# Kernel tuning notes

Measured on AMD Instinct MI355X. Metric: run time of the kernel, lower is better.

The kernel has to match this reference:

```python
import jax, jax.numpy as jnp
import numpy as np

HID = 2048
HEADS = 16
HD = HID // HEADS  # 128


def setup_inputs() -> dict:
    key = jax.random.key(0)
    ks = jax.random.split(key, 9)
    s = 0.02
    return {
        "hidden_state": jax.random.normal(ks[0], (2, 2048, HID), dtype=jnp.float32),
        "Wq": jax.random.normal(ks[1], (HID, HID), dtype=jnp.float32) * s,
        "bq": jnp.zeros((HID,), dtype=jnp.float32),
        "Wk": jax.random.normal(ks[2], (HID, HD), dtype=jnp.float32) * s,
        "bk": jnp.zeros((HD,), dtype=jnp.float32),
        "Wv": jax.random.normal(ks[3], (HID, HD), dtype=jnp.float32) * s,
        "bv": jnp.zeros((HD,), dtype=jnp.float32),
        "Wo": jax.random.normal(ks[4], (HID, HID), dtype=jnp.float32) * s,
        "bo": jnp.zeros((HID,), dtype=jnp.float32),
    }


def reference(hidden_state, Wq, bq, Wk, bk, Wv, bv, Wo, bo):
    bs, seq, _ = hidden_state.shape
    # Q: [b, s, H, hd] -> per-head; K,V: single shared head [b, s, hd]
    q = (hidden_state @ Wq + bq).reshape(bs, seq, HEADS, HD)
    k = hidden_state @ Wk + bk  # [b, s, hd]
    v = hidden_state @ Wv + bv  # [b, s, hd]
    scale = 1.0 / jnp.sqrt(jnp.float32(HD))
    # scores: [b, h, s_q, s_k] against shared K head
    scores = jnp.einsum("bqhd,bkd->bhqk", q, k) * scale
    attn = jax.nn.softmax(scores, axis=-1)
    out = jnp.einsum("bhqk,bkd->bqhd", attn, v)  # [b, s, h, hd]
    out = out.reshape(bs, seq, HID)
    return out @ Wo + bo
```

## Files before the change

### kernel.cpp

```cpp
#include <hip/hip_runtime.h>
#include <math.h>

#define HIDN 2048
#define NHEADS 16
#define HDIM 128
#define SEQ 2048
#define NB 2

#define C2 0.12751744154f

typedef __bf16 bf16x8 __attribute__((ext_vector_type(8)));
typedef float f32x4 __attribute__((ext_vector_type(4)));

__device__ __forceinline__ unsigned short f32_to_bf16(float f) {
  unsigned int u = __float_as_uint(f);
  u += 0x7FFFu + ((u >> 16) & 1u);
  return (unsigned short)(u >> 16);
}

__device__ __forceinline__ unsigned pack_bf16x2(float a, float b) {
  return (unsigned)f32_to_bf16(a) | ((unsigned)f32_to_bf16(b) << 16);
}

__device__ __forceinline__ unsigned pack_bf16x2_trunc(float a, float b) {
  return __builtin_amdgcn_perm(__float_as_uint(b), __float_as_uint(a), 0x07060302u);
}

__device__ __forceinline__ void gload_lds16(const void* g, void* l) {
  __builtin_amdgcn_global_load_lds(
      (__attribute__((address_space(1))) void*)(g),
      (__attribute__((address_space(3))) void*)(l), 16, 0, 0);
}

__global__ __launch_bounds__(256) void cast_f32_bf16(
    const float* __restrict__ in, unsigned short* __restrict__ out, int n4) {
  int i = blockIdx.x * blockDim.x + threadIdx.x;
  if (i >= n4) return;
  float4 v = ((const float4*)in)[i];
  ushort4 o;
  o.x = f32_to_bf16(v.x); o.y = f32_to_bf16(v.y);
  o.z = f32_to_bf16(v.z); o.w = f32_to_bf16(v.w);
  ((ushort4*)out)[i] = o;
}

__global__ __launch_bounds__(256) void wtrans_big(
    const float* __restrict__ wq, unsigned short* __restrict__ dq,
    const float* __restrict__ wo, unsigned short* __restrict__ do_) {
  __shared__ float tile[32][33];
  const float* src = blockIdx.z ? wo : wq;
  unsigned short* dst = blockIdx.z ? do_ : dq;
  const float m = blockIdx.z ? 1.0f : C2;
  int c0 = blockIdx.x * 32, r0 = blockIdx.y * 32;
  int tx = threadIdx.x & 31, ty = threadIdx.x >> 5;
#pragma unroll
  for (int i = 0; i < 32; i += 8)
    tile[ty + i][tx] = src[(size_t)(r0 + ty + i) * 2048 + c0 + tx];
  __syncthreads();
#pragma unroll
  for (int i = 0; i < 32; i += 8)
    dst[(size_t)(c0 + ty + i) * 2048 + r0 + tx] = f32_to_bf16(tile[tx][ty + i] * m);
}

__global__ __launch_bounds__(256) void wtrans_small(
    const float* __restrict__ wk, const float* __restrict__ wv,
    unsigned short* __restrict__ dk, unsigned short* __restrict__ dv,
    const float* __restrict__ bq, const float* __restrict__ bk,
    const float* __restrict__ bv, float* __restrict__ biasout) {
  __shared__ float tile[32][33];
  const float* src = blockIdx.z ? wv : wk;
  unsigned short* dst = blockIdx.z ? dv : dk;
  int c0 = blockIdx.x * 32, r0 = blockIdx.y * 32;
  int tx = threadIdx.x & 31, ty = threadIdx.x >> 5;
#pragma unroll
  for (int i = 0; i < 32; i += 8)
    tile[ty + i][tx] = src[(size_t)(r0 + ty + i) * 128 + c0 + tx];
  __syncthreads();
#pragma unroll
  for (int i = 0; i < 32; i += 8)
    dst[(size_t)(c0 + ty + i) * 2048 + r0 + tx] = f32_to_bf16(tile[tx][ty + i]);
  if (blockIdx.z == 0) {
    int lb = blockIdx.y * 4 + blockIdx.x;
    if (lb < 9) {
      int i = lb * 256 + threadIdx.x;
      if (i < 2304)
        biasout[i] = (i < 2048) ? bq[i] * C2
                                : ((i < 2176) ? bk[i - 2048] : bv[i - 2176]);
    }
  }
}

__global__ __launch_bounds__(256) void vtrans(
    const unsigned short* __restrict__ qkv, unsigned short* __restrict__ vt) {
  __shared__ unsigned short tile[32][33];
  const unsigned short* src = qkv + (size_t)blockIdx.z * SEQ * 2304 + 2176;
  unsigned short* dst = vt + (size_t)blockIdx.z * 128 * SEQ;
  int c0 = blockIdx.x * 32, r0 = blockIdx.y * 32;
  int tx = threadIdx.x & 31, ty = threadIdx.x >> 5;
#pragma unroll
  for (int i = 0; i < 32; i += 8)
    tile[ty + i][tx] = src[(size_t)(r0 + ty + i) * 2304 + c0 + tx];
  __syncthreads();
  const int s = r0 + tx;
  const int col = (s & ~63) | (((s >> 5) & 1) * 32 + ((s >> 2) & 3) * 8 +
                               ((s >> 4) & 1) * 4 + (s & 3));
#pragma unroll
  for (int i = 0; i < 32; i += 8)
    dst[(size_t)(c0 + ty + i) * SEQ + col] = tile[tx][ty + i];
}

template <int BN>
__global__ __launch_bounds__(256) void gemm_bt(
    const unsigned short* __restrict__ A,
    const unsigned short* __restrict__ BT,
    const float* __restrict__ bias,
    void* __restrict__ C, int K, int ldc, int outBf16) {
  constexpr int NT = BN / 32;
  __shared__ unsigned short As[128 * 64];
  __shared__ unsigned short Bs[BN * 64];
  const int tid = threadIdx.x;
  const int lane = tid & 63;
  const int wave = tid >> 6;
  const int wr = wave >> 1, wc = wave & 1;
  const int ml = lane & 15, quad = lane >> 4;
  const long bm = (long)blockIdx.x * 128;
  const long bn = (long)blockIdx.y * BN;

  const f32x4 zero4 = {0.f, 0.f, 0.f, 0.f};
  f32x4 acc[4][NT];
#pragma unroll
  for (int mt = 0; mt < 4; ++mt)
#pragma unroll
    for (int nt = 0; nt < NT; ++nt) acc[mt][nt] = zero4;

  const int srow = lane >> 3;
  const int scol = ((lane & 7) ^ srow) * 8;

  for (int k0 = 0; k0 < K; k0 += 64) {
    __syncthreads();
#pragma unroll
    for (int r = 0; r < 4; ++r) {
      const int rowb = r * 32 + wave * 8;
      gload_lds16(A + (bm + rowb + srow) * (long)K + k0 + scol, &As[rowb * 64]);
    }
#pragma unroll
    for (int r = 0; r < NT; ++r) {
      const int rowb = r * 32 + wave * 8;
      gload_lds16(BT + (bn + rowb + srow) * (long)K + k0 + scol, &Bs[rowb * 64]);
    }
    __syncthreads();
#pragma unroll
    for (int kk = 0; kk < 64; kk += 32) {
      const int g0 = (kk >> 3) + quad;
      bf16x8 af[4], bf[NT];
#pragma unroll
      for (int mt = 0; mt < 4; ++mt)
        af[mt] = *(const bf16x8*)&As[(wr * 64 + mt * 16 + ml) * 64 +
                                     ((g0 ^ (ml & 7)) << 3)];
#pragma unroll
      for (int nt = 0; nt < NT; ++nt)
        bf[nt] = *(const bf16x8*)&Bs[(wc * (BN / 2) + nt * 16 + ml) * 64 +
                                     ((g0 ^ (ml & 7)) << 3)];
#pragma unroll
      for (int mt = 0; mt < 4; ++mt)
#pragma unroll
        for (int nt = 0; nt < NT; ++nt)
          acc[mt][nt] = __builtin_amdgcn_mfma_f32_16x16x32_bf16(
              af[mt], bf[nt], acc[mt][nt], 0, 0, 0);
    }
  }

#pragma unroll
  for (int mt = 0; mt < 4; ++mt) {
#pragma unroll
    for (int nt = 0; nt < NT; ++nt) {
      const long col = bn + wc * (BN / 2) + nt * 16 + ml;
      const float bval = bias ? bias[col] : 0.f;
#pragma unroll
      for (int r = 0; r < 4; ++r) {
        const long row = bm + wr * 64 + mt * 16 + quad * 4 + r;
        const float v = acc[mt][nt][r] + bval;
        if (outBf16)
          ((unsigned short*)C)[row * ldc + col] = f32_to_bf16(v);
        else
          ((float*)C)[row * ldc + col] = v;
      }
    }
  }
}

__global__ __launch_bounds__(256, 2) void mqa_attn(
    const unsigned short* __restrict__ qkv,
    const unsigned short* __restrict__ vt,
    unsigned short* __restrict__ outp) {
  __shared__ unsigned short Ks[2][64 * 128];
  __shared__ unsigned short VTs[2][128 * 64];

  const int lane = threadIdx.x & 63;
  const int wave = threadIdx.x >> 6;
  const int ml = lane & 15, quad = lane >> 4;
  const int h = blockIdx.y, b = blockIdx.z;
  const long q0 = (long)blockIdx.x * 128;
  const long base = (long)b * SEQ;

  bf16x8 aq[2][4];
#pragma unroll
  for (int n = 0; n < 2; ++n) {
    const unsigned short* qrow =
        qkv + (base + q0 + wave * 32 + n * 16 + ml) * 2304 + h * 128;
#pragma unroll
    for (int ks = 0; ks < 4; ++ks)
      aq[n][ks] = *(const bf16x8*)(qrow + ks * 32 + quad * 8);
  }

  const f32x4 zero4 = {0.f, 0.f, 0.f, 0.f};
  f32x4 o[8][2];
#pragma unroll
  for (int mt2 = 0; mt2 < 8; ++mt2)
#pragma unroll
    for (int n = 0; n < 2; ++n) o[mt2][n] = zero4;
  f32x4 o9[2] = {zero4, zero4};

  bf16x8 ones_af;
  {
    union { unsigned u[4]; bf16x8 v; } cv;
    const unsigned w = (ml == 0) ? 0x3F803F80u : 0u;
    cv.u[0] = w; cv.u[1] = w; cv.u[2] = w; cv.u[3] = w;
    ones_af = cv.v;
  }

  const int srowK = lane >> 4;
  const int scolK = ((lane & 15) ^ (wave * 4 + srowK)) * 8;
  const int srowV = lane >> 3;
  const int scolV = ((lane & 7) ^ srowV) * 8;
  const unsigned short* kp = qkv + (base + srowK) * 2304 + 2048 + scolK;
  const unsigned short* vp = vt + ((long)b * 128 + srowV) * SEQ + scolV;

  auto stage = [&](int buf, int ktn) {
    const unsigned short* kpp = kp + (long)ktn * (64 * 2304);
    const unsigned short* vpp = vp + ktn * 64;
#pragma unroll
    for (int r = 0; r < 4; ++r) {
      const int rowb = r * 16 + wave * 4;
      gload_lds16(kpp + (long)rowb * 2304, &Ks[buf][rowb * 128]);
    }
#pragma unroll
    for (int r = 0; r < 4; ++r) {
      const int rowb = r * 32 + wave * 8;
      gload_lds16(vpp + (long)rowb * SEQ, &VTs[buf][rowb * 64]);
    }
  };

  stage(0, 0);

  for (int kt = 0; kt < SEQ / 64; ++kt) {
    const int cur = kt & 1;
    __syncthreads();
    if (kt < SEQ / 64 - 1) stage(cur ^ 1, kt + 1);

    f32x4 s[4][2];
#pragma unroll
    for (int mt = 0; mt < 4; ++mt)
#pragma unroll
      for (int n = 0; n < 2; ++n) s[mt][n] = zero4;
#pragma unroll
    for (int ks = 0; ks < 4; ++ks) {
#pragma unroll
      for (int mt = 0; mt < 4; ++mt) {
        bf16x8 ak = *(const bf16x8*)&Ks[cur][(mt * 16 + ml) * 128 +
                                            (((ks * 4 + quad) ^ ml) << 3)];
#pragma unroll
        for (int n = 0; n < 2; ++n)
          s[mt][n] = __builtin_amdgcn_mfma_f32_16x16x32_bf16(
              ak, aq[n][ks], s[mt][n], 0, 0, 0);
      }
    }

    unsigned pk[2][4][2];
#pragma unroll
    for (int mt = 0; mt < 4; ++mt)
#pragma unroll
      for (int n = 0; n < 2; ++n) {
        const float p0 = __builtin_amdgcn_exp2f(s[mt][n][0]);
        const float p1 = __builtin_amdgcn_exp2f(s[mt][n][1]);
        const float p2 = __builtin_amdgcn_exp2f(s[mt][n][2]);
        const float p3 = __builtin_amdgcn_exp2f(s[mt][n][3]);
        pk[n][mt][0] = pack_bf16x2_trunc(p0, p1);
        pk[n][mt][1] = pack_bf16x2_trunc(p2, p3);
      }

#pragma unroll
    for (int ks2 = 0; ks2 < 2; ++ks2) {
      bf16x8 bp[2];
#pragma unroll
      for (int n = 0; n < 2; ++n) {
        union { unsigned u[4]; bf16x8 v; } cv;
        cv.u[0] = pk[n][2 * ks2][0];
        cv.u[1] = pk[n][2 * ks2][1];
        cv.u[2] = pk[n][2 * ks2 + 1][0];
        cv.u[3] = pk[n][2 * ks2 + 1][1];
        bp[n] = cv.v;
      }
#pragma unroll
      for (int n = 0; n < 2; ++n)
        o9[n] = __builtin_amdgcn_mfma_f32_16x16x32_bf16(
            ones_af, bp[n], o9[n], 0, 0, 0);
#pragma unroll
      for (int mt2 = 0; mt2 < 8; ++mt2) {
        bf16x8 av = *(const bf16x8*)&VTs[cur][(mt2 * 16 + ml) * 64 +
                                             (((ks2 * 4 + quad) ^ (ml & 7)) << 3)];
#pragma unroll
        for (int n = 0; n < 2; ++n)
          o[mt2][n] = __builtin_amdgcn_mfma_f32_16x16x32_bf16(
              av, bp[n], o[mt2][n], 0, 0, 0);
      }
    }
  }

  float inv[2];
#pragma unroll
  for (int n = 0; n < 2; ++n)
    inv[n] = 1.f / __shfl(o9[n][0], ml);

#pragma unroll
  for (int n = 0; n < 2; ++n) {
    const long row = base + q0 + wave * 32 + n * 16 + ml;
#pragma unroll
    for (int mt2 = 0; mt2 < 8; ++mt2) {
      uint2 w;
      w.x = pack_bf16x2(o[mt2][n][0] * inv[n], o[mt2][n][1] * inv[n]);
      w.y = pack_bf16x2(o[mt2][n][2] * inv[n], o[mt2][n][3] * inv[n]);
      *(uint2*)&outp[row * HIDN + h * HDIM + mt2 * 16 + quad * 4] = w;
    }
  }
}

extern "C" void kernel_launch(void* const* d_in, const int* in_sizes, int n_in,
                              void* d_out, int out_size, void* d_ws, size_t ws_size,
                              hipStream_t stream) {
  const float* hidden = (const float*)d_in[0];
  const float* Wq = (const float*)d_in[1];
  const float* bq = (const float*)d_in[2];
  const float* Wk = (const float*)d_in[3];
  const float* bk = (const float*)d_in[4];
  const float* Wv = (const float*)d_in[5];
  const float* bv = (const float*)d_in[6];
  const float* Wo = (const float*)d_in[7];
  const float* bo = (const float*)d_in[8];
  float* out = (float*)d_out;

  char* ws = (char*)d_ws;
  const size_t MB = 1u << 20;
  unsigned short* hb    = (unsigned short*)(ws);
  unsigned short* attn  = hb;
  unsigned short* wqkvT = (unsigned short*)(ws + 16 * MB);
  unsigned short* woT   = (unsigned short*)(ws + 25 * MB);
  unsigned short* qkv   = (unsigned short*)(ws + 33 * MB);
  unsigned short* vt    = (unsigned short*)(ws + 51 * MB);
  float* biasqkv        = (float*)(ws + 52 * MB);

  cast_f32_bf16<<<8192, 256, 0, stream>>>(hidden, hb, (NB * SEQ * HIDN) / 4);
  wtrans_big<<<dim3(64, 64, 2), 256, 0, stream>>>(Wq, wqkvT, Wo, woT);
  wtrans_small<<<dim3(4, 64, 2), 256, 0, stream>>>(
      Wk, Wv, wqkvT + (size_t)2048 * 2048, wqkvT + (size_t)2176 * 2048,
      bq, bk, bv, biasqkv);

  gemm_bt<96><<<dim3(32, 24), 256, 0, stream>>>(hb, wqkvT, biasqkv, qkv, 2048, 2304, 1);

  vtrans<<<dim3(4, 64, 2), 256, 0, stream>>>(qkv, vt);

  mqa_attn<<<dim3(SEQ / 128, NHEADS, NB), 256, 0, stream>>>(qkv, vt, attn);

  gemm_bt<128><<<dim3(32, 16), 256, 0, stream>>>(attn, woT, bo, out, 2048, 2048, 0);
}
```

Before: 280.4 us.

## Replace GEMM with 256x256 double-buffered pipelined MFMA kernel with grid swizzle

Swaps the single-buffered 128xBN GEMM for a 512-thread, 256x256-tile kernel. It double-buffers LDS and interleaves global-to-LDS loads for the next k-tile with MFMA work on the current one, using explicit waitcnt, barriers and setprio. It also remaps block IDs for XCD-aware locality. The larger tiles cut global traffic per FLOP, but the grid drops to 144/128 blocks on a 256-CU device, so many CUs sit idle and LDS use per block goes up.

```diff
diff --git a/kernel.cpp b/kernel.cpp
--- a/kernel.cpp
+++ b/kernel.cpp
@@ -108,81 +108,156 @@
     dst[(size_t)(c0 + ty + i) * SEQ + col] = tile[tx][ty + i];
 }
 
-template <int BN>
-__global__ __launch_bounds__(256) void gemm_bt(
+template <int NBY, int LDC, int OUTBF16>
+__global__ __launch_bounds__(512, 2) void gemm256(
     const unsigned short* __restrict__ A,
     const unsigned short* __restrict__ BT,
     const float* __restrict__ bias,
-    void* __restrict__ C, int K, int ldc, int outBf16) {
-  constexpr int NT = BN / 32;
-  __shared__ unsigned short As[128 * 64];
-  __shared__ unsigned short Bs[BN * 64];
+    void* __restrict__ C, int K) {
+  __shared__ unsigned short As[2][256 * 64];
+  __shared__ unsigned short Bs[2][256 * 64];
   const int tid = threadIdx.x;
   const int lane = tid & 63;
   const int wave = tid >> 6;
-  const int wr = wave >> 1, wc = wave & 1;
+  const int wr = wave >> 2;
+  const int wc = wave & 3;
   const int ml = lane & 15, quad = lane >> 4;
-  const long bm = (long)blockIdx.x * 128;
-  const long bn = (long)blockIdx.y * BN;
+
+  const int orig = blockIdx.x;
+  const int qx = gridDim.x >> 3;
+  const int lid = (orig & 7) * qx + (orig >> 3);
+  const long bm = (long)(lid / NBY) * 256;
+  const long bn = (long)(lid % NBY) * 256;
+
+  const int srow = tid >> 3;
+  const int scol = ((tid & 7) ^ (srow & 7)) * 8;
+  const unsigned short* Ag = A + (bm + srow) * (long)K + scol;
+  const unsigned short* Bg = BT + (bn + srow) * (long)K + scol;
 
   const f32x4 zero4 = {0.f, 0.f, 0.f, 0.f};
-  f32x4 acc[4][NT];
-#pragma unroll
-  for (int mt = 0; mt < 4; ++mt)
-#pragma unroll
-    for (int nt = 0; nt < NT; ++nt) acc[mt][nt] = zero4;
-
-  const int srow = lane >> 3;
-  const int scol = ((lane & 7) ^ srow) * 8;
-
-  for (int k0 = 0; k0 < K; k0 += 64) {
-    __syncthreads();
-#pragma unroll
-    for (int r = 0; r < 4; ++r) {
-      const int rowb = r * 32 + wave * 8;
-      gload_lds16(A + (bm + rowb + srow) * (long)K + k0 + scol, &As[rowb * 64]);
-    }
-#pragma unroll
-    for (int r = 0; r < NT; ++r) {
-      const int rowb = r * 32 + wave * 8;
-      gload_lds16(BT + (bn + rowb + srow) * (long)K + k0 + scol, &Bs[rowb * 64]);
-    }
-    __syncthreads();
-#pragma unroll
-    for (int kk = 0; kk < 64; kk += 32) {
-      const int g0 = (kk >> 3) + quad;
-      bf16x8 af[4], bf[NT];
-#pragma unroll
-      for (int mt = 0; mt < 4; ++mt)
-        af[mt] = *(const bf16x8*)&As[(wr * 64 + mt * 16 + ml) * 64 +
-                                     ((g0 ^ (ml & 7)) << 3)];
-#pragma unroll
-      for (int nt = 0; nt < NT; ++nt)
-        bf[nt] = *(const bf16x8*)&Bs[(wc * (BN / 2) + nt * 16 + ml) * 64 +
-                                     ((g0 ^ (ml & 7)) << 3)];
-#pragma unroll
-      for (int mt = 0; mt < 4; ++mt)
-#pragma unroll
-        for (int nt = 0; nt < NT; ++nt)
-          acc[mt][nt] = __builtin_amdgcn_mfma_f32_16x16x32_bf16(
-              af[mt], bf[nt], acc[mt][nt], 0, 0, 0);
-    }
-  }
-
-#pragma unroll
-  for (int mt = 0; mt < 4; ++mt) {
-#pragma unroll
-    for (int nt = 0; nt < NT; ++nt) {
-      const long col = bn + wc * (BN / 2) + nt * 16 + ml;
+  f32x4 acc[8][4];
+#pragma unroll
+  for (int mt = 0; mt < 8; ++mt)
+#pragma unroll
+    for (int nt = 0; nt < 4; ++nt) acc[mt][nt] = zero4;
+
+  bf16x8 bfr[4][2];
+
+#define STA(buf, koff, R0) \
+  gload_lds16(Ag + (long)(R0) * K + (koff), &As[buf][((R0) + 8 * wave) * 64])
+#define STB(buf, koff, R0) \
+  gload_lds16(Bg + (long)(R0) * K + (koff), &Bs[buf][((R0) + 8 * wave) * 64])
+#define RDA(buf, mt, kk) \
+  (*(const bf16x8*)&As[buf][(wr * 128 + (mt) * 16 + ml) * 64 + \
+                            ((((kk) * 4 + quad) ^ (ml & 7)) << 3)])
+#define RDB(buf, nt, kk) \
+  (*(const bf16x8*)&Bs[buf][(wc * 64 + (nt) * 16 + ml) * 64 + \
+                            ((((kk) * 4 + quad) ^ (ml & 7)) << 3)])
+
+  STB(0, 0, 0); STB(0, 0, 64); STB(0, 0, 128); STB(0, 0, 192);
+  STA(0, 0, 0); STA(0, 0, 128); STA(0, 0, 64); STA(0, 0, 192);
+  asm volatile("s_waitcnt vmcnt(2)" ::: "memory");
+  __builtin_amdgcn_s_barrier();
+
+  const int NT = K >> 6;
+  for (int t = 0; t < NT - 1; ++t) {
+    const int buf = t & 1, nbuf = buf ^ 1;
+    const long kn = (long)(t + 1) << 6;
+#pragma unroll
+    for (int q = 0; q < 4; ++q) {
+      __builtin_amdgcn_sched_barrier(0);
+      bf16x8 afr[2][2];
+      if (q == 0) {
+#pragma unroll
+        for (int nt = 0; nt < 4; ++nt)
+#pragma unroll
+          for (int kk = 0; kk < 2; ++kk) bfr[nt][kk] = RDB(buf, nt, kk);
+      }
+#pragma unroll
+      for (int j = 0; j < 2; ++j)
+#pragma unroll
+        for (int kk = 0; kk < 2; ++kk) afr[j][kk] = RDA(buf, 2 * q + j, kk);
+      if (q == 0) { STB(nbuf, kn, 0); STB(nbuf, kn, 64); }
+      if (q == 1) {
+        STB(nbuf, kn, 128); STB(nbuf, kn, 192);
+        asm volatile("s_waitcnt vmcnt(4)" ::: "memory");
+      }
+      if (q == 2) { STA(nbuf, kn, 0); STA(nbuf, kn, 128); }
+      if (q == 3) {
+        STA(nbuf, kn, 64); STA(nbuf, kn, 192);
+        asm volatile("s_waitcnt vmcnt(2)" ::: "memory");
+      }
+      __builtin_amdgcn_sched_barrier(0);
+      __builtin_amdgcn_s_barrier();
+      __builtin_amdgcn_sched_barrier(0);
+      __builtin_amdgcn_s_setprio(1);
+#pragma unroll
+      for (int j = 0; j < 2; ++j)
+#pragma unroll
+        for (int nt = 0; nt < 4; ++nt)
+#pragma unroll
+          for (int kk = 0; kk < 2; ++kk)
+            acc[2 * q + j][nt] = __builtin_amdgcn_mfma_f32_16x16x32_bf16(
+                afr[j][kk], bfr[nt][kk], acc[2 * q + j][nt], 0, 0, 0);
+      __builtin_amdgcn_s_setprio(0);
+      __builtin_amdgcn_sched_barrier(0);
+      __builtin_amdgcn_s_barrier();
+    }
+  }
+
+  {
+    const int buf = (NT - 1) & 1;
+#pragma unroll
+    for (int q = 0; q < 4; ++q) {
+      __builtin_amdgcn_sched_barrier(0);
+      bf16x8 afr[2][2];
+      if (q == 0) {
+#pragma unroll
+        for (int nt = 0; nt < 4; ++nt)
+#pragma unroll
+          for (int kk = 0; kk < 2; ++kk) bfr[nt][kk] = RDB(buf, nt, kk);
+      }
+#pragma unroll
+      for (int j = 0; j < 2; ++j)
+#pragma unroll
+        for (int kk = 0; kk < 2; ++kk) afr[j][kk] = RDA(buf, 2 * q + j, kk);
+      if (q == 1) asm volatile("s_waitcnt vmcnt(0)" ::: "memory");
+      __builtin_amdgcn_sched_barrier(0);
+      __builtin_amdgcn_s_barrier();
+      __builtin_amdgcn_sched_barrier(0);
+      __builtin_amdgcn_s_setprio(1);
+#pragma unroll
+      for (int j = 0; j < 2; ++j)
+#pragma unroll
+        for (int nt = 0; nt < 4; ++nt)
+#pragma unroll
+          for (int kk = 0; kk < 2; ++kk)
+            acc[2 * q + j][nt] = __builtin_amdgcn_mfma_f32_16x16x32_bf16(
+                afr[j][kk], bfr[nt][kk], acc[2 * q + j][nt], 0, 0, 0);
+      __builtin_amdgcn_s_setprio(0);
+      __builtin_amdgcn_sched_barrier(0);
+      __builtin_amdgcn_s_barrier();
+    }
+  }
+#undef STA
+#undef STB
+#undef RDA
+#undef RDB
+
+#pragma unroll
+  for (int mt = 0; mt < 8; ++mt) {
+#pragma unroll
+    for (int nt = 0; nt < 4; ++nt) {
+      const long col = bn + wc * 64 + nt * 16 + ml;
       const float bval = bias ? bias[col] : 0.f;
 #pragma unroll
       for (int r = 0; r < 4; ++r) {
-        const long row = bm + wr * 64 + mt * 16 + quad * 4 + r;
+        const long row = bm + wr * 128 + mt * 16 + quad * 4 + r;
         const float v = acc[mt][nt][r] + bval;
-        if (outBf16)
-          ((unsigned short*)C)[row * ldc + col] = f32_to_bf16(v);
+        if (OUTBF16)
+          ((unsigned short*)C)[row * LDC + col] = f32_to_bf16(v);
         else
-          ((float*)C)[row * ldc + col] = v;
+          ((float*)C)[row * LDC + col] = v;
       }
     }
   }
@@ -364,11 +439,11 @@
       Wk, Wv, wqkvT + (size_t)2048 * 2048, wqkvT + (size_t)2176 * 2048,
       bq, bk, bv, biasqkv);
 
-  gemm_bt<96><<<dim3(32, 24), 256, 0, stream>>>(hb, wqkvT, biasqkv, qkv, 2048, 2304, 1);
+  gemm256<9, 2304, 1><<<dim3(144), 512, 0, stream>>>(hb, wqkvT, biasqkv, qkv, 2048);
 
   vtrans<<<dim3(4, 64, 2), 256, 0, stream>>>(qkv, vt);
 
   mqa_attn<<<dim3(SEQ / 128, NHEADS, NB), 256, 0, stream>>>(qkv, vt, attn);
 
-  gemm_bt<128><<<dim3(32, 16), 256, 0, stream>>>(attn, woT, bo, out, 2048, 2048, 0);
-}
+  gemm256<8, 2048, 0><<<dim3(128), 512, 0, stream>>>(attn, woT, bo, out, 2048);
+}
```

New measurement: 308.9 us. 10.1% more time.

## Fuse prep kernels into one launch and add triple-buffered output-projection GEMM

Applied to the files above, without the earlier changes.

Merges the hidden-state cast and the two weight-transpose kernels into a single prep launch with block-index dispatch, which removes launch overhead. Replaces the output projection GEMM with a new 512-thread kernel. It uses 128x256 tiles, a three-stage LDS buffer filled by direct global-to-LDS loads, and XOR-swizzled LDS layout. It also splits each k-step into two MFMA phases separated by barriers, with setprio and a block-index remap for L2 locality. The new GEMM uses much more LDS per block and hardcodes shape assumptions through its template parameters.

```diff
diff --git a/kernel.cpp b/kernel.cpp
--- a/kernel.cpp
+++ b/kernel.cpp
@@ -32,59 +32,65 @@
       (__attribute__((address_space(3))) void*)(l), 16, 0, 0);
 }
 
-__global__ __launch_bounds__(256) void cast_f32_bf16(
-    const float* __restrict__ in, unsigned short* __restrict__ out, int n4) {
-  int i = blockIdx.x * blockDim.x + threadIdx.x;
-  if (i >= n4) return;
-  float4 v = ((const float4*)in)[i];
-  ushort4 o;
-  o.x = f32_to_bf16(v.x); o.y = f32_to_bf16(v.y);
-  o.z = f32_to_bf16(v.z); o.w = f32_to_bf16(v.w);
-  ((ushort4*)out)[i] = o;
-}
-
-__global__ __launch_bounds__(256) void wtrans_big(
+__global__ __launch_bounds__(256) void prep(
+    const float* __restrict__ hidden, unsigned short* __restrict__ hb,
     const float* __restrict__ wq, unsigned short* __restrict__ dq,
-    const float* __restrict__ wo, unsigned short* __restrict__ do_) {
-  __shared__ float tile[32][33];
-  const float* src = blockIdx.z ? wo : wq;
-  unsigned short* dst = blockIdx.z ? do_ : dq;
-  const float m = blockIdx.z ? 1.0f : C2;
-  int c0 = blockIdx.x * 32, r0 = blockIdx.y * 32;
-  int tx = threadIdx.x & 31, ty = threadIdx.x >> 5;
-#pragma unroll
-  for (int i = 0; i < 32; i += 8)
-    tile[ty + i][tx] = src[(size_t)(r0 + ty + i) * 2048 + c0 + tx];
-  __syncthreads();
-#pragma unroll
-  for (int i = 0; i < 32; i += 8)
-    dst[(size_t)(c0 + ty + i) * 2048 + r0 + tx] = f32_to_bf16(tile[tx][ty + i] * m);
-}
-
-__global__ __launch_bounds__(256) void wtrans_small(
+    const float* __restrict__ wo, unsigned short* __restrict__ do_,
     const float* __restrict__ wk, const float* __restrict__ wv,
     unsigned short* __restrict__ dk, unsigned short* __restrict__ dv,
     const float* __restrict__ bq, const float* __restrict__ bk,
     const float* __restrict__ bv, float* __restrict__ biasout) {
   __shared__ float tile[32][33];
-  const float* src = blockIdx.z ? wv : wk;
-  unsigned short* dst = blockIdx.z ? dv : dk;
-  int c0 = blockIdx.x * 32, r0 = blockIdx.y * 32;
-  int tx = threadIdx.x & 31, ty = threadIdx.x >> 5;
-#pragma unroll
-  for (int i = 0; i < 32; i += 8)
-    tile[ty + i][tx] = src[(size_t)(r0 + ty + i) * 128 + c0 + tx];
-  __syncthreads();
-#pragma unroll
-  for (int i = 0; i < 32; i += 8)
-    dst[(size_t)(c0 + ty + i) * 2048 + r0 + tx] = f32_to_bf16(tile[tx][ty + i]);
-  if (blockIdx.z == 0) {
-    int lb = blockIdx.y * 4 + blockIdx.x;
-    if (lb < 9) {
-      int i = lb * 256 + threadIdx.x;
-      if (i < 2304)
-        biasout[i] = (i < 2048) ? bq[i] * C2
-                                : ((i < 2176) ? bk[i - 2048] : bv[i - 2176]);
+  const int blk = blockIdx.x;
+  const int tx = threadIdx.x & 31, ty = threadIdx.x >> 5;
+  if (blk < 8192) {
+    int i = blk * 256 + threadIdx.x;
+    float4 v = ((const float4*)hidden)[i];
+    ushort4 o;
+    o.x = f32_to_bf16(v.x); o.y = f32_to_bf16(v.y);
+    o.z = f32_to_bf16(v.z); o.w = f32_to_bf16(v.w);
+    ((ushort4*)hb)[i] = o;
+    return;
+  }
+  if (blk < 16384) {
+    int r = blk - 8192;
+    const int z = r >> 12; r &= 4095;
+    const int bx = r & 63, by = r >> 6;
+    const float* src = z ? wo : wq;
+    unsigned short* dst = z ? do_ : dq;
+    const float m = z ? 1.0f : C2;
+    const int c0 = bx * 32, r0 = by * 32;
+#pragma unroll
+    for (int i = 0; i < 32; i += 8)
+      tile[ty + i][tx] = src[(size_t)(r0 + ty + i) * 2048 + c0 + tx];
+    __syncthreads();
+#pragma unroll
+    for (int i = 0; i < 32; i += 8)
+      dst[(size_t)(c0 + ty + i) * 2048 + r0 + tx] = f32_to_bf16(tile[tx][ty + i] * m);
+    return;
+  }
+  {
+    int r = blk - 16384;
+    const int z = r >> 8; r &= 255;
+    const int bx = r & 3, by = r >> 2;
+    const float* src = z ? wv : wk;
+    unsigned short* dst = z ? dv : dk;
+    const int c0 = bx * 32, r0 = by * 32;
+#pragma unroll
+    for (int i = 0; i < 32; i += 8)
+      tile[ty + i][tx] = src[(size_t)(r0 + ty + i) * 128 + c0 + tx];
+    __syncthreads();
+#pragma unroll
+    for (int i = 0; i < 32; i += 8)
+      dst[(size_t)(c0 + ty + i) * 2048 + r0 + tx] = f32_to_bf16(tile[tx][ty + i]);
+    if (z == 0) {
+      int lb = by * 4 + bx;
+      if (lb < 9) {
+        int i = lb * 256 + threadIdx.x;
+        if (i < 2304)
+          biasout[i] = (i < 2048) ? bq[i] * C2
+                                  : ((i < 2176) ? bk[i - 2048] : bv[i - 2176]);
+      }
     }
   }
 }
@@ -188,6 +194,135 @@
   }
 }
 
+template <int NBY, int LDC, int OUTBF16>
+__global__ __launch_bounds__(512, 2) void gemm_ko(
+    const unsigned short* __restrict__ A,
+    const unsigned short* __restrict__ BT,
+    const float* __restrict__ bias,
+    void* __restrict__ C, int K) {
+  __shared__ unsigned short As[3][128 * 64];
+  __shared__ unsigned short Bs[3][256 * 64];
+  const int tid = threadIdx.x;
+  const int lane = tid & 63;
+  const int wave = tid >> 6;
+  const int wr = wave >> 2;
+  const int wc = wave & 3;
+  const int ml = lane & 15, quad = lane >> 4;
+
+  const int orig = blockIdx.x;
+  const int qx = gridDim.x >> 3;
+  const int lid = (orig & 7) * qx + (orig >> 3);
+  const long bm = (long)(lid / NBY) * 128;
+  const long bn = (long)(lid % NBY) * 256;
+
+  const int srow = tid >> 3;
+  const int scol = ((tid & 7) ^ (srow & 7)) * 8;
+  const unsigned short* Ag = A + (bm + srow) * (long)K + scol;
+  const unsigned short* Bg = BT + (bn + srow) * (long)K + scol;
+
+  const f32x4 zero4 = {0.f, 0.f, 0.f, 0.f};
+  f32x4 acc[4][4];
+#pragma unroll
+  for (int mt = 0; mt < 4; ++mt)
+#pragma unroll
+    for (int nt = 0; nt < 4; ++nt) acc[mt][nt] = zero4;
+
+  bf16x8 bfr[4][2];
+
+#define STA(buf, koff, R0) \
+  gload_lds16(Ag + (long)(R0) * K + (koff), &As[buf][((R0) + 8 * wave) * 64])
+#define STB(buf, koff, R0) \
+  gload_lds16(Bg + (long)(R0) * K + (koff), &Bs[buf][((R0) + 8 * wave) * 64])
+#define RDA(buf, mt, kk) \
+  (*(const bf16x8*)&As[buf][(wr * 64 + (mt) * 16 + ml) * 64 + \
+                            ((((kk) * 4 + quad) ^ (ml & 7)) << 3)])
+#define RDB(buf, nt, kk) \
+  (*(const bf16x8*)&Bs[buf][(wc * 64 + (nt) * 16 + ml) * 64 + \
+                            ((((kk) * 4 + quad) ^ (ml & 7)) << 3)])
+
+  STB(0, 0, 0); STB(0, 0, 64); STB(0, 0, 128); STB(0, 0, 192);
+  STA(0, 0, 0); STA(0, 0, 64);
+  STB(1, 64, 0); STB(1, 64, 64); STB(1, 64, 128); STB(1, 64, 192);
+  STA(1, 64, 0); STA(1, 64, 64);
+  asm volatile("s_waitcnt vmcnt(6)" ::: "memory");
+  __builtin_amdgcn_s_barrier();
+
+  const int NT = K >> 6;
+  for (int t = 0; t < NT; ++t) {
+    const int buf = t % 3, sb = (t + 2) % 3;
+    const long kn = (long)(t + 2) << 6;
+    const bool st = (t + 2) < NT;
+    __builtin_amdgcn_sched_barrier(0);
+    bf16x8 afr[2][2];
+#pragma unroll
+    for (int nt = 0; nt < 4; ++nt)
+#pragma unroll
+      for (int kk = 0; kk < 2; ++kk) bfr[nt][kk] = RDB(buf, nt, kk);
+#pragma unroll
+    for (int j = 0; j < 2; ++j)
+#pragma unroll
+      for (int kk = 0; kk < 2; ++kk) afr[j][kk] = RDA(buf, j, kk);
+    if (st) { STB(sb, kn, 0); STB(sb, kn, 64); STB(sb, kn, 128); STB(sb, kn, 192); }
+    __builtin_amdgcn_s_barrier();
+    __builtin_amdgcn_s_setprio(1);
+#pragma unroll
+    for (int j = 0; j < 2; ++j)
+#pragma unroll
+      for (int nt = 0; nt < 4; ++nt)
+#pragma unroll
+        for (int kk = 0; kk < 2; ++kk)
+          acc[j][nt] = __builtin_amdgcn_mfma_f32_16x16x32_bf16(
+              afr[j][kk], bfr[nt][kk], acc[j][nt], 0, 0, 0);
+    __builtin_amdgcn_s_setprio(0);
+    __builtin_amdgcn_s_barrier();
+    __builtin_amdgcn_sched_barrier(0);
+#pragma unroll
+    for (int j = 0; j < 2; ++j)
+#pragma unroll
+      for (int kk = 0; kk < 2; ++kk) afr[j][kk] = RDA(buf, 2 + j, kk);
+    if (st) {
+      STA(sb, kn, 0); STA(sb, kn, 64);
+      asm volatile("s_waitcnt vmcnt(6)" ::: "memory");
+    } else if (t == NT - 2) {
+      asm volatile("s_waitcnt vmcnt(0)" ::: "memory");
+    }
+    __builtin_amdgcn_s_barrier();
+    __builtin_amdgcn_s_setprio(1);
+#pragma unroll
+    for (int j = 0; j < 2; ++j)
+#pragma unroll
+      for (int nt = 0; nt < 4; ++nt)
+#pragma unroll
+        for (int kk = 0; kk < 2; ++kk)
+          acc[2 + j][nt] = __builtin_amdgcn_mfma_f32_16x16x32_bf16(
+              afr[j][kk], bfr[nt][kk], acc[2 + j][nt], 0, 0, 0);
+    __builtin_amdgcn_s_setprio(0);
+    __builtin_amdgcn_s_barrier();
+  }
+#undef STA
+#undef STB
+#undef RDA
+#undef RDB
+
+#pragma unroll
+  for (int mt = 0; mt < 4; ++mt) {
+#pragma unroll
+    for (int nt = 0; nt < 4; ++nt) {
+      const long col = bn + wc * 64 + nt * 16 + ml;
+      const float bval = bias ? bias[col] : 0.f;
+#pragma unroll
+      for (int r = 0; r < 4; ++r) {
+        const long row = bm + wr * 64 + mt * 16 + quad * 4 + r;
+        const float v = acc[mt][nt][r] + bval;
+        if (OUTBF16)
+          ((unsigned short*)C)[row * LDC + col] = f32_to_bf16(v);
+        else
+          ((float*)C)[row * LDC + col] = v;
+      }
+    }
+  }
+}
+
 __global__ __launch_bounds__(256, 2) void mqa_attn(
     const unsigned short* __restrict__ qkv,
     const unsigned short* __restrict__ vt,
@@ -358,11 +493,10 @@
   unsigned short* vt    = (unsigned short*)(ws + 51 * MB);
   float* biasqkv        = (float*)(ws + 52 * MB);
 
-  cast_f32_bf16<<<8192, 256, 0, stream>>>(hidden, hb, (NB * SEQ * HIDN) / 4);
-  wtrans_big<<<dim3(64, 64, 2), 256, 0, stream>>>(Wq, wqkvT, Wo, woT);
-  wtrans_small<<<dim3(4, 64, 2), 256, 0, stream>>>(
-      Wk, Wv, wqkvT + (size_t)2048 * 2048, wqkvT + (size_t)2176 * 2048,
-      bq, bk, bv, biasqkv);
+  prep<<<16896, 256, 0, stream>>>(hidden, hb, Wq, wqkvT, Wo, woT, Wk, Wv,
+                                  wqkvT + (size_t)2048 * 2048,
+                                  wqkvT + (size_t)2176 * 2048,
+                                  bq, bk, bv, biasqkv);
 
   gemm_bt<96><<<dim3(32, 24), 256, 0, stream>>>(hb, wqkvT, biasqkv, qkv, 2048, 2304, 1);
 
@@ -370,5 +504,5 @@
 
   mqa_attn<<<dim3(SEQ / 128, NHEADS, NB), 256, 0, stream>>>(qkv, vt, attn);
 
-  gemm_bt<128><<<dim3(32, 16), 256, 0, stream>>>(attn, woT, bo, out, 2048, 2048, 0);
-}
+  gemm_ko<8, 2048, 0><<<dim3(256), 512, 0, stream>>>(attn, woT, bo, out, 2048);
+}
```

Measured after the change: 280.5 us. About the same (+0.0%).
